# Optimization experiments

Hardware: AMD Instinct MI355X
Metric: run time of the kernel (lower is better)

Reference implementation:

```python
import jax, jax.numpy as jnp
import numpy as np

B, IN_CH, OFF_CH, OUT_CH, H, W, K = 2, 256, 256, 256, 128, 128, 3
KK = K * K


def setup_inputs() -> dict:
    key = jax.random.key(0)
    k0, k1, k2, k3, k4 = jax.random.split(key, 5)
    x = jax.random.normal(k0, (B, IN_CH, H, W), jnp.float32)
    off = jax.random.normal(k1, (B, OFF_CH, H, W), jnp.float32)
    # xavier_uniform-scale (approximated with scaled normals)
    s_off = (2.0 / (OFF_CH + 3 * KK)) ** 0.5
    w_off = jax.random.normal(k2, (3 * KK, OFF_CH, 1, 1), jnp.float32) * s_off
    b_off = jnp.zeros((3 * KK,), jnp.float32)  # init_offset zeros the bias
    s_w = (2.0 / (IN_CH * KK + OUT_CH * KK)) ** 0.5
    w = jax.random.normal(k3, (OUT_CH, IN_CH, K, K), jnp.float32) * s_w
    b = jax.random.normal(k4, (OUT_CH,), jnp.float32) * 0.01
    return {"x": x, "off": off, "w_off": w_off, "b_off": b_off, "w": w, "b": b}


def _bilinear_gather(x, ys, xs):
    # Zero outside the image (per DCNv2 corner validity check).
    Bb, C, Hin, Win = x.shape
    x_flat = x.reshape(Bb, C, Hin * Win)
    y0 = jnp.floor(ys)
    x0 = jnp.floor(xs)
    wy1 = ys - y0
    wx1 = xs - x0
    wy0 = 1.0 - wy1
    wx0 = 1.0 - wx1

    def corner(yc, xc, wgt):
        valid = (yc >= 0) & (yc <= Hin - 1) & (xc >= 0) & (xc <= Win - 1)
        yi = jnp.clip(yc, 0, Hin - 1).astype(jnp.int32)
        xi = jnp.clip(xc, 0, Win - 1).astype(jnp.int32)
        idx = (yi * Win + xi)[:, None, :]  # [B,1,N]
        v = jnp.take_along_axis(x_flat, idx, axis=2)  # [B,C,N]
        return v * (wgt * valid.astype(x.dtype))[:, None, :]

    return (corner(y0, x0, wy0 * wx0) + corner(y0, x0 + 1, wy0 * wx1)
            + corner(y0 + 1, x0, wy1 * wx0) + corner(y0 + 1, x0 + 1, wy1 * wx1))


def reference(x, off, w_off, b_off, w, b):
    Bb, Cin, Hin, Win = x.shape
    pad = K // 2
    # 1x1 offset/mask conv
    out = jnp.einsum('oc,bchw->bohw', w_off[:, :, 0, 0], off) + b_off[None, :, None, None]
    o1, o2, mask = jnp.split(out, 3, axis=1)
    offset = jnp.concatenate([o1, o2], axis=1)  # [B, 2*KK, H, W]
    mask = jax.nn.sigmoid(mask)                 # [B, KK, H, W]
    # DCNv2 reads offset channels interleaved: (dy_k, dx_k) for kernel point k
    offs = offset.reshape(Bb, KK, 2, Hin, Win)
    dy, dx = offs[:, :, 0], offs[:, :, 1]       # [B, KK, H, W]
    kh = (jnp.arange(KK) // K).astype(x.dtype)
    kw = (jnp.arange(KK) % K).astype(x.dtype)
    iy = jnp.arange(Hin, dtype=x.dtype)
    ix = jnp.arange(Win, dtype=x.dtype)
    ys = iy[None, None, :, None] + (kh - pad)[None, :, None, None] + dy
    xs = ix[None, None, None, :] + (kw - pad)[None, :, None, None] + dx
    val = _bilinear_gather(x, ys.reshape(Bb, -1), xs.reshape(Bb, -1))  # [B,C,KK*H*W]
    val = val.reshape(Bb, Cin, KK, Hin, Win) * mask[:, None]
    y = jnp.einsum('ock,bckhw->bohw', w.reshape(w.shape[0], Cin, KK), val)
    y = y + b[None, :, None, None]
    return jax.nn.relu(y)
```

## Files before the change

kernel.cpp:

```cpp
#include <hip/hip_runtime.h>
#include <stdint.h>

#define HH 128
#define WW 128
#define CIN 256
#define OCH 256
#define HW (HH*WW)

typedef __attribute__((ext_vector_type(8))) short bf16x8;
typedef __attribute__((ext_vector_type(16))) float f32x16;

static __device__ __forceinline__ uint16_t f2bf(float f) {
  uint32_t u = __builtin_bit_cast(uint32_t, f);
  u += 0x7FFFu + ((u >> 16) & 1u);
  return (uint16_t)(u >> 16);
}
static __device__ __forceinline__ float bf2f(uint16_t h) {
  uint32_t u = ((uint32_t)h) << 16;
  return __builtin_bit_cast(float, u);
}

#define LBAR() asm volatile("s_waitcnt lgkmcnt(0)\ns_barrier" ::: "memory")

__global__ void pack_w_kernel(const float* __restrict__ w, uint16_t* __restrict__ wpk) {
  int i = blockIdx.x * 256 + threadIdx.x;
  int ci = i & 7;
  int oc = (i >> 3) & 255;
  int c8 = (i >> 11) & 31;
  int k  = i >> 16;
  int c = c8 * 8 + ci;
  wpk[i] = f2bf(w[(oc * 256 + c) * 9 + k]);
}

__global__ void transpose_kernel(const float* __restrict__ x, uint32_t* __restrict__ xt) {
  __shared__ float tile[64][65];
  int wg = blockIdx.x;
  int b  = wg >> 10;
  int r  = wg & 1023;
  int pt = r >> 2, ct = r & 3;
  int p0 = pt * 64, c0 = ct * 64;
  int t = threadIdx.x;
  int px4 = (t & 15) * 4;
#pragma unroll
  for (int i = 0; i < 4; ++i) {
    int cl = i * 16 + (t >> 4);
    const float4 v = *(const float4*)&x[(size_t)(b * CIN + c0 + cl) * HW + p0 + px4];
    tile[cl][px4 + 0] = v.x; tile[cl][px4 + 1] = v.y;
    tile[cl][px4 + 2] = v.z; tile[cl][px4 + 3] = v.w;
  }
  __syncthreads();
  int c2 = t & 31, pr = t >> 5;
#pragma unroll
  for (int i = 0; i < 8; ++i) {
    int pl = i * 8 + pr;
    uint32_t lo = f2bf(tile[2 * c2][pl]);
    uint32_t hi = f2bf(tile[2 * c2 + 1][pl]);
    xt[(size_t)(b * HW + p0 + pl) * 128 + (c0 >> 1) + c2] = lo | (hi << 16);
  }
}

__global__ __launch_bounds__(256) void offc_kernel(const float* __restrict__ off,
                                                   const float* __restrict__ w_off,
                                                   const float* __restrict__ b_off,
                                                   float* __restrict__ offs) {
  __shared__ float wl[27 * 256];
  __shared__ float red[3][64][29];
  int t = threadIdx.x;
  for (int r = t; r < 27 * 256; r += 256) wl[r] = w_off[r];
  int pxl = t & 63, q = t >> 6;
  int px = blockIdx.x * 64 + pxl;
  int b = px >> 14, yx = px & 16383;
  float acc[27];
#pragma unroll
  for (int jj = 0; jj < 27; ++jj) acc[jj] = 0.f;
  const float* op = off + (size_t)b * CIN * HW + yx;
  int cbase = q * 64;
  __syncthreads();
  for (int c = 0; c < 64; c += 4) {
    float v0 = op[(size_t)(cbase + c + 0) * HW];
    float v1 = op[(size_t)(cbase + c + 1) * HW];
    float v2 = op[(size_t)(cbase + c + 2) * HW];
    float v3 = op[(size_t)(cbase + c + 3) * HW];
    const float* wr = wl + cbase + c;
#pragma unroll
    for (int jj = 0; jj < 27; ++jj) {
      acc[jj] = fmaf(wr[jj * 256 + 0], v0, acc[jj]);
      acc[jj] = fmaf(wr[jj * 256 + 1], v1, acc[jj]);
      acc[jj] = fmaf(wr[jj * 256 + 2], v2, acc[jj]);
      acc[jj] = fmaf(wr[jj * 256 + 3], v3, acc[jj]);
    }
  }
  if (q > 0) {
#pragma unroll
    for (int jj = 0; jj < 27; ++jj) red[q - 1][pxl][jj] = acc[jj];
  }
  __syncthreads();
  if (q == 0) {
    float fin[27];
#pragma unroll
    for (int jj = 0; jj < 27; ++jj)
      acc[jj] += b_off[jj] + red[0][pxl][jj] + red[1][pxl][jj] + red[2][pxl][jj];
#pragma unroll
    for (int k = 0; k < 9; ++k) {
      fin[3 * k + 0] = acc[2 * k];
      fin[3 * k + 1] = acc[2 * k + 1];
      fin[3 * k + 2] = 1.f / (1.f + __expf(-acc[18 + k]));
    }
#pragma unroll
    for (int jj = 0; jj < 27; ++jj) red[0][pxl][jj] = fin[jj];
  }
  __syncthreads();
  float* obase = offs + (size_t)blockIdx.x * 64 * 27;
  for (int r = t; r < 64 * 27; r += 256) {
    int p = r / 27, e = r - p * 27;
    obase[r] = red[0][p][e];
  }
}

__global__ __launch_bounds__(256, 4) void main_kernel(
    const uint32_t* __restrict__ xt, const float* __restrict__ offs,
    const uint16_t* __restrict__ wpk, const float* __restrict__ bias,
    float* __restrict__ out) {
  __shared__ struct __align__(16) { unsigned char A[2][32 * 512]; float offs_l[32 * 27]; } sm;

  int wg = blockIdx.x;
  wg = (wg & 7) * 128 + (wg >> 3);
  int b = wg >> 9;
  int tile = wg & 511;
  int y0 = (tile >> 4) * 4, x0 = (tile & 15) * 8;

  int tid = threadIdx.x;
  int lane = tid & 63;
  int wv = tid >> 6;
  int l31 = lane & 31, g = lane >> 5;

  {
    int base = b * HW + y0 * WW + x0;
    for (int r = tid; r < 32 * 27; r += 256) {
      int pyl = r / 216;
      int rem = r - pyl * 216;
      sm.offs_l[r] = offs[(size_t)(base + pyl * WW) * 27 + rem];
    }
  }
  f32x16 acc[2] = {};

  const int hw = tid >> 5;
  const int j = tid & 31;
  const uint4* xt4 = (const uint4*)xt;
  const uint4* wp4 = (const uint4*)wpk;
  const int pb = b * HW;
  const uint32_t rswz = (uint32_t)(l31 << 4);
  const int oc0 = wv * 64 + l31;

  auto issue = [&](int kk, int i, float* wt, uint4* q) {
    int px = hw * 4 + i;
    int kh = kk / 3 - 1, kw = kk % 3 - 1;
    float dy = sm.offs_l[px * 27 + kk * 3 + 0];
    float dx = sm.offs_l[px * 27 + kk * 3 + 1];
    float m  = sm.offs_l[px * 27 + kk * 3 + 2];
    float ys = (float)(y0 + (px >> 3) + kh) + dy;
    float xs = (float)(x0 + (px & 7) + kw) + dx;
    float yf = floorf(ys), xf = floorf(xs);
    float wy1 = ys - yf, wx1 = xs - xf;
    float wy0 = 1.f - wy1, wx0 = 1.f - wx1;
    int iy0 = (int)yf, ix0 = (int)xf;
    int iy1 = iy0 + 1, ix1 = ix0 + 1;
    float vy0 = (iy0 >= 0 && iy0 < HH) ? 1.f : 0.f;
    float vy1 = (iy1 >= 0 && iy1 < HH) ? 1.f : 0.f;
    float vx0 = (ix0 >= 0 && ix0 < WW) ? 1.f : 0.f;
    float vx1 = (ix1 >= 0 && ix1 < WW) ? 1.f : 0.f;
    wt[0] = wy0 * wx0 * vy0 * vx0 * m;
    wt[1] = wy0 * wx1 * vy0 * vx1 * m;
    wt[2] = wy1 * wx0 * vy1 * vx0 * m;
    wt[3] = wy1 * wx1 * vy1 * vx1 * m;
    int cy0 = iy0 < 0 ? 0 : (iy0 > HH - 1 ? HH - 1 : iy0);
    int cy1 = iy1 < 0 ? 0 : (iy1 > HH - 1 ? HH - 1 : iy1);
    int cx0 = ix0 < 0 ? 0 : (ix0 > WW - 1 ? WW - 1 : ix0);
    int cx1 = ix1 < 0 ? 0 : (ix1 > WW - 1 ? WW - 1 : ix1);
    q[0] = xt4[(size_t)(pb + cy0 * WW + cx0) * 32 + j];
    q[1] = xt4[(size_t)(pb + cy0 * WW + cx1) * 32 + j];
    q[2] = xt4[(size_t)(pb + cy1 * WW + cx0) * 32 + j];
    q[3] = xt4[(size_t)(pb + cy1 * WW + cx1) * 32 + j];
  };

  auto commit = [&](int i, const float* wt, const uint4* q, int buf) {
    int px = hw * 4 + i;
    uint32_t u0[4] = {q[0].x, q[0].y, q[0].z, q[0].w};
    uint32_t u1[4] = {q[1].x, q[1].y, q[1].z, q[1].w};
    uint32_t u2[4] = {q[2].x, q[2].y, q[2].z, q[2].w};
    uint32_t u3[4] = {q[3].x, q[3].y, q[3].z, q[3].w};
    uint32_t ow[4];
#pragma unroll
    for (int qd = 0; qd < 4; ++qd) {
      float lo = wt[0] * bf2f((uint16_t)u0[qd]) + wt[1] * bf2f((uint16_t)u1[qd])
               + wt[2] * bf2f((uint16_t)u2[qd]) + wt[3] * bf2f((uint16_t)u3[qd]);
      float hi = wt[0] * bf2f((uint16_t)(u0[qd] >> 16)) + wt[1] * bf2f((uint16_t)(u1[qd] >> 16))
               + wt[2] * bf2f((uint16_t)(u2[qd] >> 16)) + wt[3] * bf2f((uint16_t)(u3[qd] >> 16));
      ow[qd] = (uint32_t)f2bf(lo) | ((uint32_t)f2bf(hi) << 16);
    }
    *(uint4*)(&sm.A[buf][px * 512 + ((j * 16) ^ (px << 4))]) =
        make_uint4(ow[0], ow[1], ow[2], ow[3]);
  };

  auto mfma_half = [&](int kk, int h, int buf) {
    __builtin_amdgcn_s_setprio(1);
#pragma unroll
    for (int chunk = 0; chunk < 4; ++chunk) {
#pragma unroll
      for (int cs = 0; cs < 2; ++cs) {
        int ch = h * 4 + chunk;
        int boff = (ch * 64 + cs * 32 + g * 16) ^ rswz;
        uint4 ua = *(const uint4*)(&sm.A[buf][l31 * 512 + boff]);
        int bidx = kk * 8192 + (ch * 4 + cs * 2 + g) * 256;
        uint4 ub0 = wp4[bidx + oc0];
        uint4 ub1 = wp4[bidx + oc0 + 32];
        bf16x8 a  = __builtin_bit_cast(bf16x8, ua);
        bf16x8 b0 = __builtin_bit_cast(bf16x8, ub0);
        bf16x8 b1 = __builtin_bit_cast(bf16x8, ub1);
        acc[0] = __builtin_amdgcn_mfma_f32_32x32x16_bf16(a, b0, acc[0], 0, 0, 0);
        acc[1] = __builtin_amdgcn_mfma_f32_32x32x16_bf16(a, b1, acc[1], 0, 0, 0);
      }
    }
    __builtin_amdgcn_s_setprio(0);
  };

  LBAR();

  {
    float wt0[4], wt1[4];
    uint4 q0[4], q1[4];
#pragma unroll
    for (int ip = 0; ip < 2; ++ip) {
      issue(0, 2 * ip + 0, wt0, q0);
      issue(0, 2 * ip + 1, wt1, q1);
      commit(2 * ip + 0, wt0, q0, 0);
      commit(2 * ip + 1, wt1, q1, 0);
    }
  }

#pragma unroll 1
  for (int k = 0; k < 9; ++k) {
    int buf = k & 1, nbuf = buf ^ 1;
    float wt0[4], wt1[4];
    uint4 q0[4], q1[4];
    if (k < 8) { issue(k + 1, 0, wt0, q0); issue(k + 1, 1, wt1, q1); }
    LBAR();
    mfma_half(k, 0, buf);
    if (k < 8) {
      commit(0, wt0, q0, nbuf);
      commit(1, wt1, q1, nbuf);
      issue(k + 1, 2, wt0, q0);
      issue(k + 1, 3, wt1, q1);
    }
    mfma_half(k, 1, buf);
    if (k < 8) {
      commit(2, wt0, q0, nbuf);
      commit(3, wt1, q1, nbuf);
    }
  }

  float bv0 = bias[wv * 64 + l31];
  float bv1 = bias[wv * 64 + 32 + l31];
#pragma unroll
  for (int tn = 0; tn < 2; ++tn) {
    int oc = wv * 64 + tn * 32 + l31;
    float bv = tn ? bv1 : bv0;
#pragma unroll
    for (int r = 0; r < 16; ++r) {
      int row = (r & 3) + 8 * (r >> 2) + 4 * g;
      int y = y0 + (row >> 3), x = x0 + (row & 7);
      float v = acc[tn][r] + bv;
      out[((size_t)(b * OCH + oc) << 14) + (y << 7) + x] = fmaxf(v, 0.f);
    }
  }
}

extern "C" void kernel_launch(void* const* d_in, const int* in_sizes, int n_in,
                              void* d_out, int out_size, void* d_ws, size_t ws_size,
                              hipStream_t stream) {
  const float* x     = (const float*)d_in[0];
  const float* off   = (const float*)d_in[1];
  const float* w_off = (const float*)d_in[2];
  const float* b_off = (const float*)d_in[3];
  const float* w     = (const float*)d_in[4];
  const float* bias  = (const float*)d_in[5];
  float* out = (float*)d_out;
  char* ws = (char*)d_ws;
  uint32_t* xt   = (uint32_t*)ws;
  float*    offs = (float*)(ws + 16777216);
  uint16_t* wpk  = (uint16_t*)(ws + 16777216 + 3538944);

  pack_w_kernel<<<2304, 256, 0, stream>>>(w, wpk);
  transpose_kernel<<<2048, 256, 0, stream>>>(x, xt);
  offc_kernel<<<512, 256, 0, stream>>>(off, w_off, b_off, offs);
  main_kernel<<<1024, 256, 0, stream>>>(xt, offs, wpk, bias, out);
}
```

Measured before the change: 301.2 us.

## Merge prep kernels into one launch and enlarge main-kernel pixel tile

The three preprocessing kernels (bf16 transpose of x, weight packing, offset conv) become one multi-role launch selected by block index. The offset conv now splits channels across 4 adjacent lanes and reduces with shuffles, with padded shared weights read as float4, instead of a shared-memory reduction. The main kernel moves to 512-thread blocks covering 64 pixels (4x16) so each wave's weight fragment is reused across two pixel halves, halving the number of blocks. This costs larger shared memory per block and possibly lower occupancy.

```diff
diff --git a/kernel.cpp b/kernel.cpp
--- a/kernel.cpp
+++ b/kernel.cpp
@@ -22,144 +22,144 @@
 
 #define LBAR() asm volatile("s_waitcnt lgkmcnt(0)\ns_barrier" ::: "memory")
 
-__global__ void pack_w_kernel(const float* __restrict__ w, uint16_t* __restrict__ wpk) {
-  int i = blockIdx.x * 256 + threadIdx.x;
-  int ci = i & 7;
-  int oc = (i >> 3) & 255;
-  int c8 = (i >> 11) & 31;
-  int k  = i >> 16;
-  int c = c8 * 8 + ci;
-  wpk[i] = f2bf(w[(oc * 256 + c) * 9 + k]);
-}
-
-__global__ void transpose_kernel(const float* __restrict__ x, uint32_t* __restrict__ xt) {
-  __shared__ float tile[64][65];
-  int wg = blockIdx.x;
-  int b  = wg >> 10;
-  int r  = wg & 1023;
-  int pt = r >> 2, ct = r & 3;
-  int p0 = pt * 64, c0 = ct * 64;
+#define TR_BLOCKS 2048
+#define PK_BLOCKS 2304
+#define OC_BLOCKS 512
+
+__global__ __launch_bounds__(256) void prep_kernel(
+    const float* __restrict__ x, uint32_t* __restrict__ xt,
+    const float* __restrict__ w, uint16_t* __restrict__ wpk,
+    const float* __restrict__ off, const float* __restrict__ w_off,
+    const float* __restrict__ b_off, float* __restrict__ offs) {
+  __shared__ __align__(16) char smraw[27 * 4 * 68 * 4];
+  int bid = blockIdx.x;
   int t = threadIdx.x;
-  int px4 = (t & 15) * 4;
-#pragma unroll
-  for (int i = 0; i < 4; ++i) {
-    int cl = i * 16 + (t >> 4);
-    const float4 v = *(const float4*)&x[(size_t)(b * CIN + c0 + cl) * HW + p0 + px4];
-    tile[cl][px4 + 0] = v.x; tile[cl][px4 + 1] = v.y;
-    tile[cl][px4 + 2] = v.z; tile[cl][px4 + 3] = v.w;
-  }
-  __syncthreads();
-  int c2 = t & 31, pr = t >> 5;
-#pragma unroll
-  for (int i = 0; i < 8; ++i) {
-    int pl = i * 8 + pr;
-    uint32_t lo = f2bf(tile[2 * c2][pl]);
-    uint32_t hi = f2bf(tile[2 * c2 + 1][pl]);
-    xt[(size_t)(b * HW + p0 + pl) * 128 + (c0 >> 1) + c2] = lo | (hi << 16);
-  }
-}
-
-__global__ __launch_bounds__(256) void offc_kernel(const float* __restrict__ off,
-                                                   const float* __restrict__ w_off,
-                                                   const float* __restrict__ b_off,
-                                                   float* __restrict__ offs) {
-  __shared__ float wl[27 * 256];
-  __shared__ float red[3][64][29];
-  int t = threadIdx.x;
-  for (int r = t; r < 27 * 256; r += 256) wl[r] = w_off[r];
-  int pxl = t & 63, q = t >> 6;
-  int px = blockIdx.x * 64 + pxl;
-  int b = px >> 14, yx = px & 16383;
-  float acc[27];
-#pragma unroll
-  for (int jj = 0; jj < 27; ++jj) acc[jj] = 0.f;
-  const float* op = off + (size_t)b * CIN * HW + yx;
-  int cbase = q * 64;
-  __syncthreads();
-  for (int c = 0; c < 64; c += 4) {
-    float v0 = op[(size_t)(cbase + c + 0) * HW];
-    float v1 = op[(size_t)(cbase + c + 1) * HW];
-    float v2 = op[(size_t)(cbase + c + 2) * HW];
-    float v3 = op[(size_t)(cbase + c + 3) * HW];
-    const float* wr = wl + cbase + c;
+
+  if (bid < TR_BLOCKS) {
+    float (*tile)[65] = reinterpret_cast<float(*)[65]>(smraw);
+    int b = bid >> 10;
+    int r = bid & 1023;
+    int pt = r >> 2, ct = r & 3;
+    int p0 = pt * 64, c0 = ct * 64;
+    int px4 = (t & 15) * 4;
+#pragma unroll
+    for (int i = 0; i < 4; ++i) {
+      int cl = i * 16 + (t >> 4);
+      const float4 v = *(const float4*)&x[(size_t)(b * CIN + c0 + cl) * HW + p0 + px4];
+      tile[cl][px4 + 0] = v.x; tile[cl][px4 + 1] = v.y;
+      tile[cl][px4 + 2] = v.z; tile[cl][px4 + 3] = v.w;
+    }
+    __syncthreads();
+    int c2 = t & 31, pr = t >> 5;
+#pragma unroll
+    for (int i = 0; i < 8; ++i) {
+      int pl = i * 8 + pr;
+      uint32_t lo = f2bf(tile[2 * c2][pl]);
+      uint32_t hi = f2bf(tile[2 * c2 + 1][pl]);
+      xt[(size_t)(b * HW + p0 + pl) * 128 + (c0 >> 1) + c2] = lo | (hi << 16);
+    }
+  } else if (bid < TR_BLOCKS + PK_BLOCKS) {
+    int i = (bid - TR_BLOCKS) * 256 + t;
+    int ci = i & 7;
+    int oc = (i >> 3) & 255;
+    int c8 = (i >> 11) & 31;
+    int k  = i >> 16;
+    int c = c8 * 8 + ci;
+    wpk[i] = f2bf(w[(oc * 256 + c) * 9 + k]);
+  } else {
+    float* wl = (float*)smraw;
+    for (int r = t; r < 27 * 256; r += 256) {
+      int jj = r >> 8, rest = r & 255, cg = rest >> 6, c = rest & 63;
+      wl[(jj * 4 + cg) * 68 + c] = w_off[r];
+    }
+    __syncthreads();
+    int ob = bid - (TR_BLOCKS + PK_BLOCKS);
+    int pxl = t >> 2, cg = t & 3;
+    int px = ob * 64 + pxl;
+    int b = px >> 14, yx = px & 16383;
+    const float* op = off + (size_t)b * (CIN * HW) + (size_t)(cg * 64) * HW + yx;
+    float acc[27];
+#pragma unroll
+    for (int jj = 0; jj < 27; ++jj) acc[jj] = 0.f;
+    for (int c = 0; c < 64; c += 4) {
+      float v0 = op[(size_t)(c + 0) * HW];
+      float v1 = op[(size_t)(c + 1) * HW];
+      float v2 = op[(size_t)(c + 2) * HW];
+      float v3 = op[(size_t)(c + 3) * HW];
+#pragma unroll
+      for (int jj = 0; jj < 27; ++jj) {
+        const float4 ww = *(const float4*)&wl[(jj * 4 + cg) * 68 + c];
+        acc[jj] = fmaf(ww.x, v0, acc[jj]);
+        acc[jj] = fmaf(ww.y, v1, acc[jj]);
+        acc[jj] = fmaf(ww.z, v2, acc[jj]);
+        acc[jj] = fmaf(ww.w, v3, acc[jj]);
+      }
+    }
 #pragma unroll
     for (int jj = 0; jj < 27; ++jj) {
-      acc[jj] = fmaf(wr[jj * 256 + 0], v0, acc[jj]);
-      acc[jj] = fmaf(wr[jj * 256 + 1], v1, acc[jj]);
-      acc[jj] = fmaf(wr[jj * 256 + 2], v2, acc[jj]);
-      acc[jj] = fmaf(wr[jj * 256 + 3], v3, acc[jj]);
-    }
-  }
-  if (q > 0) {
-#pragma unroll
-    for (int jj = 0; jj < 27; ++jj) red[q - 1][pxl][jj] = acc[jj];
-  }
-  __syncthreads();
-  if (q == 0) {
+      acc[jj] += __shfl_xor(acc[jj], 1, 64);
+      acc[jj] += __shfl_xor(acc[jj], 2, 64);
+    }
     float fin[27];
 #pragma unroll
+    for (int kk = 0; kk < 9; ++kk) {
+      fin[3 * kk + 0] = acc[2 * kk + 0] + b_off[2 * kk + 0];
+      fin[3 * kk + 1] = acc[2 * kk + 1] + b_off[2 * kk + 1];
+      float mm = acc[18 + kk] + b_off[18 + kk];
+      fin[3 * kk + 2] = 1.f / (1.f + __expf(-mm));
+    }
+    float* o = offs + (size_t)px * 27;
+#pragma unroll
     for (int jj = 0; jj < 27; ++jj)
-      acc[jj] += b_off[jj] + red[0][pxl][jj] + red[1][pxl][jj] + red[2][pxl][jj];
-#pragma unroll
-    for (int k = 0; k < 9; ++k) {
-      fin[3 * k + 0] = acc[2 * k];
-      fin[3 * k + 1] = acc[2 * k + 1];
-      fin[3 * k + 2] = 1.f / (1.f + __expf(-acc[18 + k]));
-    }
-#pragma unroll
-    for (int jj = 0; jj < 27; ++jj) red[0][pxl][jj] = fin[jj];
-  }
-  __syncthreads();
-  float* obase = offs + (size_t)blockIdx.x * 64 * 27;
-  for (int r = t; r < 64 * 27; r += 256) {
-    int p = r / 27, e = r - p * 27;
-    obase[r] = red[0][p][e];
-  }
-}
-
-__global__ __launch_bounds__(256, 4) void main_kernel(
+      if ((jj & 3) == cg) o[jj] = fin[jj];
+  }
+}
+
+__global__ __launch_bounds__(512) void main_kernel(
     const uint32_t* __restrict__ xt, const float* __restrict__ offs,
     const uint16_t* __restrict__ wpk, const float* __restrict__ bias,
     float* __restrict__ out) {
-  __shared__ struct __align__(16) { unsigned char A[2][32 * 512]; float offs_l[32 * 27]; } sm;
+  __shared__ struct __align__(16) { unsigned char A[2][64 * 512]; float offs_l[64 * 27]; } sm;
 
   int wg = blockIdx.x;
-  wg = (wg & 7) * 128 + (wg >> 3);
-  int b = wg >> 9;
-  int tile = wg & 511;
-  int y0 = (tile >> 4) * 4, x0 = (tile & 15) * 8;
+  wg = (wg & 7) * 64 + (wg >> 3);
+  int b = wg >> 8;
+  int tile = wg & 255;
+  int y0 = (tile >> 3) * 4, x0 = (tile & 7) * 16;
 
   int tid = threadIdx.x;
   int lane = tid & 63;
   int wv = tid >> 6;
+  int ocg = wv & 3, ph = wv >> 2;
   int l31 = lane & 31, g = lane >> 5;
 
   {
     int base = b * HW + y0 * WW + x0;
-    for (int r = tid; r < 32 * 27; r += 256) {
-      int pyl = r / 216;
-      int rem = r - pyl * 216;
+    for (int r = tid; r < 64 * 27; r += 512) {
+      int pyl = r / 432;
+      int rem = r - pyl * 432;
       sm.offs_l[r] = offs[(size_t)(base + pyl * WW) * 27 + rem];
     }
   }
   f32x16 acc[2] = {};
 
-  const int hw = tid >> 5;
+  const int pxg = tid >> 5;
   const int j = tid & 31;
   const uint4* xt4 = (const uint4*)xt;
   const uint4* wp4 = (const uint4*)wpk;
   const int pb = b * HW;
   const uint32_t rswz = (uint32_t)(l31 << 4);
-  const int oc0 = wv * 64 + l31;
+  const int oc0 = ocg * 64 + l31;
+  const int arow = (l31 + 32 * ph) * 512;
 
   auto issue = [&](int kk, int i, float* wt, uint4* q) {
-    int px = hw * 4 + i;
+    int px = pxg * 4 + i;
     int kh = kk / 3 - 1, kw = kk % 3 - 1;
     float dy = sm.offs_l[px * 27 + kk * 3 + 0];
     float dx = sm.offs_l[px * 27 + kk * 3 + 1];
     float m  = sm.offs_l[px * 27 + kk * 3 + 2];
-    float ys = (float)(y0 + (px >> 3) + kh) + dy;
-    float xs = (float)(x0 + (px & 7) + kw) + dx;
+    float ys = (float)(y0 + (px >> 4) + kh) + dy;
+    float xs = (float)(x0 + (px & 15) + kw) + dx;
     float yf = floorf(ys), xf = floorf(xs);
     float wy1 = ys - yf, wx1 = xs - xf;
     float wy0 = 1.f - wy1, wx0 = 1.f - wx1;
@@ -184,7 +184,7 @@
   };
 
   auto commit = [&](int i, const float* wt, const uint4* q, int buf) {
-    int px = hw * 4 + i;
+    int px = pxg * 4 + i;
     uint32_t u0[4] = {q[0].x, q[0].y, q[0].z, q[0].w};
     uint32_t u1[4] = {q[1].x, q[1].y, q[1].z, q[1].w};
     uint32_t u2[4] = {q[2].x, q[2].y, q[2].z, q[2].w};
@@ -198,7 +198,7 @@
                + wt[2] * bf2f((uint16_t)(u2[qd] >> 16)) + wt[3] * bf2f((uint16_t)(u3[qd] >> 16));
       ow[qd] = (uint32_t)f2bf(lo) | ((uint32_t)f2bf(hi) << 16);
     }
-    *(uint4*)(&sm.A[buf][px * 512 + ((j * 16) ^ (px << 4))]) =
+    *(uint4*)(&sm.A[buf][px * 512 + ((j * 16) ^ ((px & 31) << 4))]) =
         make_uint4(ow[0], ow[1], ow[2], ow[3]);
   };
 
@@ -210,7 +210,7 @@
       for (int cs = 0; cs < 2; ++cs) {
         int ch = h * 4 + chunk;
         int boff = (ch * 64 + cs * 32 + g * 16) ^ rswz;
-        uint4 ua = *(const uint4*)(&sm.A[buf][l31 * 512 + boff]);
+        uint4 ua = *(const uint4*)(&sm.A[buf][arow + boff]);
         int bidx = kk * 8192 + (ch * 4 + cs * 2 + g) * 256;
         uint4 ub0 = wp4[bidx + oc0];
         uint4 ub1 = wp4[bidx + oc0 + 32];
@@ -259,16 +259,16 @@
     }
   }
 
-  float bv0 = bias[wv * 64 + l31];
-  float bv1 = bias[wv * 64 + 32 + l31];
+  float bv0 = bias[ocg * 64 + l31];
+  float bv1 = bias[ocg * 64 + 32 + l31];
 #pragma unroll
   for (int tn = 0; tn < 2; ++tn) {
-    int oc = wv * 64 + tn * 32 + l31;
+    int oc = ocg * 64 + tn * 32 + l31;
     float bv = tn ? bv1 : bv0;
 #pragma unroll
     for (int r = 0; r < 16; ++r) {
-      int row = (r & 3) + 8 * (r >> 2) + 4 * g;
-      int y = y0 + (row >> 3), x = x0 + (row & 7);
+      int row = 32 * ph + (r & 3) + 8 * (r >> 2) + 4 * g;
+      int y = y0 + (row >> 4), x = x0 + (row & 15);
       float v = acc[tn][r] + bv;
       out[((size_t)(b * OCH + oc) << 14) + (y << 7) + x] = fmaxf(v, 0.f);
     }
@@ -290,8 +290,7 @@
   float*    offs = (float*)(ws + 16777216);
   uint16_t* wpk  = (uint16_t*)(ws + 16777216 + 3538944);
 
-  pack_w_kernel<<<2304, 256, 0, stream>>>(w, wpk);
-  transpose_kernel<<<2048, 256, 0, stream>>>(x, xt);
-  offc_kernel<<<512, 256, 0, stream>>>(off, w_off, b_off, offs);
-  main_kernel<<<1024, 256, 0, stream>>>(xt, offs, wpk, bias, out);
-}
+  prep_kernel<<<TR_BLOCKS + PK_BLOCKS + OC_BLOCKS, 256, 0, stream>>>(
+      x, xt, w, wpk, off, w_off, b_off, offs);
+  main_kernel<<<512, 512, 0, stream>>>(xt, offs, wpk, bias, out);
+}
```

Measured after the change: 251.5 us. -16.5%, faster.
